# Optimization experiments

Hardware: AMD Instinct MI355X
Metric: run time of the kernel (lower is better)

Reference implementation:

```python
import jax, jax.numpy as jnp
import numpy as np
import math

SCALED = True
SUBSEQUENT_MASK = True
B, SQ, SK, D, DV = 8, 2048, 2048, 1024, 1024


def _build_mask(query_lens, key_lens, sq, sk, causal):
    # (B, Sq, Sk) boolean validity mask: rows >= q_len and cols >= k_len are masked.
    qm = jnp.arange(sq)[None, :, None] < query_lens[:, None, None]
    km = jnp.arange(sk)[None, None, :] < key_lens[:, None, None]
    mask = qm & km
    if causal:
        mask = mask & (jnp.arange(sk)[None, None, :] <= jnp.arange(sq)[None, :, None])
    return mask


def _masked_softmax(scores, mask):
    # Stable masked softmax; fully-masked rows yield exactly 0 (matches the
    # original's NaN -> 0 replacement) without producing NaNs.
    neg = jnp.finfo(scores.dtype).min
    s = jnp.where(mask, scores, neg)
    m = jnp.max(s, axis=-1, keepdims=True)
    e = jnp.where(mask, jnp.exp(s - m), jnp.zeros((), scores.dtype))
    denom = jnp.sum(e, axis=-1, keepdims=True)
    return e / jnp.where(denom == 0, jnp.ones((), scores.dtype), denom)


def setup_inputs() -> dict:
    key = jax.random.key(0)
    kq, kk, kv, kql, kkl = jax.random.split(key, 5)
    return {
        "queries": jax.random.normal(kq, (B, SQ, D), dtype=jnp.float32),
        "keys": jax.random.normal(kk, (B, SK, D), dtype=jnp.float32),
        "values": jax.random.normal(kv, (B, SK, DV), dtype=jnp.float32),
        "query_lens": jax.random.randint(kql, (B,), 1, SQ + 1),
        "key_lens": jax.random.randint(kkl, (B,), 1, SK + 1),
    }


def reference(queries, keys, values, query_lens, key_lens):
    # scores: (B, Sq, Sk)
    scores = jnp.einsum("bqd,bkd->bqk", queries, keys)
    if SCALED:
        scores = scores / math.sqrt(queries.shape[2])
    mask = _build_mask(query_lens, key_lens, queries.shape[1], keys.shape[1], SUBSEQUENT_MASK)
    weights = _masked_softmax(scores, mask)
    context = jnp.einsum("bqk,bkv->bqv", weights, values)
    return (context, weights)
```

## Files before the change

kernel.cpp:

```cpp
#include <hip/hip_runtime.h>
#include <hip/hip_bf16.h>

#define B_   8
#define SQ_  2048
#define SK_  2048
#define D_   1024
#define DV_  1024

typedef __bf16 bf16;
typedef __attribute__((ext_vector_type(4))) __bf16 bf16x4;
typedef __attribute__((ext_vector_type(8))) __bf16 bf16x8;
typedef __attribute__((ext_vector_type(4))) float  f32x4;

typedef const __attribute__((address_space(1))) void* gptr1;
typedef __attribute__((address_space(3))) void*       lptr3;

__device__ __forceinline__ void gload16(const void* g, void* l) {
    __builtin_amdgcn_global_load_lds((gptr1)g, (lptr3)l, 16, 0, 0);
}

__global__ __launch_bounds__(256)
void convert_kernel(const float* __restrict__ A, const float* __restrict__ Bm,
                    bf16* __restrict__ dA, bf16* __restrict__ dB,
                    float* __restrict__ rowsumG)
{
    if (rowsumG && blockIdx.y == 0 && blockIdx.x < 8) {
        int idx = blockIdx.x * 256 + threadIdx.x;
        float4 z = make_float4(0.f, 0.f, 0.f, 0.f);
        ((float4*)rowsumG)[idx * 2 + 0] = z;
        ((float4*)rowsumG)[idx * 2 + 1] = z;
    }
    const float* src = blockIdx.y ? Bm : A;
    bf16*        dst = blockIdx.y ? dB : dA;
    size_t i = ((size_t)blockIdx.x * 256 + threadIdx.x) * 8;
    float4 v0 = *(const float4*)(src + i);
    float4 v1 = *(const float4*)(src + i + 4);
    bf16x8 o = { (bf16)v0.x, (bf16)v0.y, (bf16)v0.z, (bf16)v0.w,
                 (bf16)v1.x, (bf16)v1.y, (bf16)v1.z, (bf16)v1.w };
    *(bf16x8*)(dst + i) = o;
}

__global__ __launch_bounds__(256)
void convVT_kernel(const float* __restrict__ V, bf16* __restrict__ VT)
{
    const int b  = blockIdx.z;
    const int k0 = blockIdx.x * 64;
    const int n0 = blockIdx.y * 64;
    __shared__ bf16 T[64][72];

    const int tid = threadIdx.x;
    #pragma unroll
    for (int i = 0; i < 4; ++i) {
        int s  = tid + i * 256;
        int r  = s >> 4;
        int c4 = (s & 15) << 2;
        float4 v = *(const float4*)(V + ((size_t)b * SK_ + (k0 + r)) * DV_ + n0 + c4);
        T[r][c4 + 0] = (bf16)v.x;
        T[r][c4 + 1] = (bf16)v.y;
        T[r][c4 + 2] = (bf16)v.z;
        T[r][c4 + 3] = (bf16)v.w;
    }
    __syncthreads();
    #pragma unroll
    for (int i = 0; i < 2; ++i) {
        int s  = tid + i * 256;
        int n  = s >> 3;
        int c8 = (s & 7) << 3;
        bf16x8 o;
        #pragma unroll
        for (int j = 0; j < 8; ++j) o[j] = T[c8 + j][n];
        *(bf16x8*)(VT + ((size_t)b * DV_ + (n0 + n)) * SK_ + k0 + c8) = o;
    }
}

__global__ __launch_bounds__(512, 4)
void scoresE_kernel(const bf16* __restrict__ Qbf, const bf16* __restrict__ Kbf,
                    const int* __restrict__ qlens, const int* __restrict__ klens,
                    bf16* __restrict__ Wbf, float* __restrict__ rowsumG)
{
    const int b  = blockIdx.z;
    const int q0 = blockIdx.y * 128;
    const int k0 = blockIdx.x * 128;
    if (k0 > q0 + 127) return;
    const int qlen = qlens[b], klen = klens[b];
    if (q0 >= qlen || k0 >= klen) return;

    __shared__ __align__(16) bf16 Qs[128][64];
    __shared__ __align__(16) bf16 Ks[128][64];
    __shared__ float rowsumL[128];

    const int tid  = threadIdx.x;
    const int lane = tid & 63;
    const int w    = tid >> 6;
    const int wq   = w >> 1, wk = w & 1;

    if (tid < 128) rowsumL[tid] = 0.f;

    const bf16* Qb = Qbf + ((size_t)b * SQ_ + q0) * D_;
    const bf16* Kb = Kbf + ((size_t)b * SK_ + k0) * D_;

    const int r0 = tid >> 3;
    const int c0 = (tid & 7) << 3;

    f32x4 acc[2][4] = {};

    for (int d0 = 0; d0 < D_; d0 += 64) {
        gload16(Qb + (size_t)r0 * D_ + d0 + c0,        &Qs[r0][c0]);
        gload16(Qb + (size_t)(r0 + 64) * D_ + d0 + c0, &Qs[r0 + 64][c0]);
        gload16(Kb + (size_t)r0 * D_ + d0 + c0,        &Ks[r0][c0]);
        gload16(Kb + (size_t)(r0 + 64) * D_ + d0 + c0, &Ks[r0 + 64][c0]);
        __syncthreads();
        #pragma unroll
        for (int kk = 0; kk < 2; ++kk) {
            const int koff = kk * 32 + ((lane >> 4) << 3);
            bf16x8 a[2], bb[4];
            #pragma unroll
            for (int m = 0; m < 2; ++m)
                a[m] = *(const bf16x8*)&Qs[32 * wq + 16 * m + (lane & 15)][koff];
            #pragma unroll
            for (int n = 0; n < 4; ++n)
                bb[n] = *(const bf16x8*)&Ks[64 * wk + 16 * n + (lane & 15)][koff];
            #pragma unroll
            for (int m = 0; m < 2; ++m)
                #pragma unroll
                for (int n = 0; n < 4; ++n)
                    acc[m][n] = __builtin_amdgcn_mfma_f32_16x16x32_bf16(a[m], bb[n], acc[m][n], 0, 0, 0);
        }
        __syncthreads();
    }

    bf16* Wrow = Wbf + ((size_t)b * SQ_ + q0) * SK_ + k0;
    const int g   = lane >> 4;
    const int cl  = lane & 15;
    const int rbl = 32 * wq + (g << 2);
    const int cbl = 64 * wk + cl;
    #pragma unroll
    for (int m = 0; m < 2; ++m) {
        #pragma unroll
        for (int r = 0; r < 4; ++r) {
            const int rl   = rbl + 16 * m + r;
            const int rowg = q0 + rl;
            float s = 0.f;
            #pragma unroll
            for (int n = 0; n < 4; ++n) {
                const int colg = k0 + cbl + 16 * n;
                float e = 0.f;
                if (rowg < qlen && colg <= rowg && colg < klen)
                    e = __expf(acc[m][n][r] * 0.03125f);
                Wrow[(size_t)rl * SK_ + cbl + 16 * n] = (bf16)e;
                s += e;
            }
            s += __shfl_xor(s, 1, 64);
            s += __shfl_xor(s, 2, 64);
            s += __shfl_xor(s, 4, 64);
            s += __shfl_xor(s, 8, 64);
            if (cl == 0) atomicAdd(&rowsumL[rl], s);
        }
    }
    __syncthreads();
    if (tid < 128) {
        float sv = rowsumL[tid];
        if (sv != 0.f) atomicAdd(&rowsumG[(size_t)b * SQ_ + q0 + tid], sv);
    }
}

__global__ __launch_bounds__(512)
void normW_kernel(const int* __restrict__ qlens, const int* __restrict__ klens,
                  const float* __restrict__ rowsumG, bf16* __restrict__ Wbf,
                  float* __restrict__ W, float* __restrict__ invG)
{
    const int b  = blockIdx.y;
    const int q0 = blockIdx.x * 64;
    const int qlen = qlens[b], klen = klens[b];
    const int tid = threadIdx.x;
    float* Wb = W + ((size_t)b * SQ_ + q0) * SK_;

    if (q0 >= qlen) {
        float4 z = make_float4(0.f, 0.f, 0.f, 0.f);
        float4* wf = (float4*)Wb;
        #pragma unroll
        for (int i = 0; i < 64; ++i) wf[tid + i * 512] = z;
        float4* bfp = (float4*)(Wbf + ((size_t)b * SQ_ + q0) * SK_);
        #pragma unroll
        for (int i = 0; i < 32; ++i) bfp[tid + i * 512] = z;
        if (tid < 64) invG[(size_t)b * SQ_ + q0 + tid] = 0.f;
        return;
    }

    const int ncols = min(klen, q0 + 64);
    const int kendB = ((ncols + 127) >> 7) << 7;

    __shared__ float invS[64];
    if (tid < 64) {
        float sv = rowsumG[(size_t)b * SQ_ + q0 + tid];
        float iv = (sv > 0.f) ? (1.f / sv) : 0.f;
        invS[tid] = iv;
        invG[(size_t)b * SQ_ + q0 + tid] = iv;
    }
    __syncthreads();

    const int r  = tid >> 3;
    const int c8 = tid & 7;
    const float iv = invS[r];
    const bf16* Erow = Wbf + ((size_t)b * SQ_ + q0 + r) * SK_;
    float* Wrow = Wb + (size_t)r * SK_;
    for (int j = 0; j < 64; ++j) {
        int col = (c8 + j * 8) << 2;
        float4 o;
        if (col < kendB) {
            bf16x4 e4 = *(const bf16x4*)&Erow[col];
            o = make_float4((float)e4[0] * iv, (float)e4[1] * iv,
                            (float)e4[2] * iv, (float)e4[3] * iv);
        } else {
            o = make_float4(0.f, 0.f, 0.f, 0.f);
        }
        *(float4*)&Wrow[col] = o;
    }
}

__global__ __launch_bounds__(512, 4)
void context_bf_kernel(const bf16* __restrict__ Wbf, const bf16* __restrict__ VT,
                       const int* __restrict__ qlens, const int* __restrict__ klens,
                       const float* __restrict__ invG, float* __restrict__ Out)
{
    const int b  = blockIdx.z;
    const int q0 = blockIdx.y * 128;
    const int n0 = blockIdx.x * 128;
    const int tid  = threadIdx.x;
    const int qlen = qlens[b];

    float* Ob = Out + (size_t)b * SQ_ * DV_;
    if (q0 >= qlen) {
        float4 z = make_float4(0.f, 0.f, 0.f, 0.f);
        #pragma unroll
        for (int i = 0; i < 8; ++i) {
            int s  = tid + i * 512;
            int r  = s >> 5;
            int c4 = (s & 31) << 2;
            *(float4*)(Ob + (size_t)(q0 + r) * DV_ + n0 + c4) = z;
        }
        return;
    }

    const int klen = klens[b];
    const int kend = min(q0 + 128, (klen + 63) & ~63);
    const int nk   = kend >> 6;

    __shared__ __align__(16) bf16 Ws[128][64];
    __shared__ __align__(16) bf16 Vs[128][64];

    const int lane = tid & 63;
    const int w    = tid >> 6;
    const int wq   = w >> 1, wn = w & 1;

    const bf16* Wb = Wbf + (size_t)b * SQ_ * SK_ + (size_t)q0 * SK_;
    const bf16* Vb = VT  + (size_t)b * DV_ * SK_ + (size_t)n0 * SK_;

    const int r0 = tid >> 3;
    const int c0 = (tid & 7) << 3;

    f32x4 acc[2][4] = {};

    for (int it = 0; it < nk; ++it) {
        const int kk0 = it * 64;
        gload16(Wb + (size_t)r0 * SK_ + kk0 + c0,        &Ws[r0][c0]);
        gload16(Wb + (size_t)(r0 + 64) * SK_ + kk0 + c0, &Ws[r0 + 64][c0]);
        gload16(Vb + (size_t)r0 * SK_ + kk0 + c0,        &Vs[r0][c0]);
        gload16(Vb + (size_t)(r0 + 64) * SK_ + kk0 + c0, &Vs[r0 + 64][c0]);
        __syncthreads();
        #pragma unroll
        for (int kk = 0; kk < 2; ++kk) {
            const int koff = kk * 32 + ((lane >> 4) << 3);
            bf16x8 a[2], bb[4];
            #pragma unroll
            for (int m = 0; m < 2; ++m)
                a[m] = *(const bf16x8*)&Ws[32 * wq + 16 * m + (lane & 15)][koff];
            #pragma unroll
            for (int n = 0; n < 4; ++n)
                bb[n] = *(const bf16x8*)&Vs[64 * wn + 16 * n + (lane & 15)][koff];
            #pragma unroll
            for (int m = 0; m < 2; ++m)
                #pragma unroll
                for (int n = 0; n < 4; ++n)
                    acc[m][n] = __builtin_amdgcn_mfma_f32_16x16x32_bf16(a[m], bb[n], acc[m][n], 0, 0, 0);
        }
        __syncthreads();
    }

    const float* invB = invG + (size_t)b * SQ_;
    const int rb = q0 + 32 * wq + ((lane >> 4) << 2);
    const int cb = n0 + 64 * wn + (lane & 15);
    #pragma unroll
    for (int m = 0; m < 2; ++m) {
        #pragma unroll
        for (int r = 0; r < 4; ++r) {
            const float iv = invB[rb + 16 * m + r];
            #pragma unroll
            for (int n = 0; n < 4; ++n)
                Ob[(size_t)(rb + 16 * m + r) * DV_ + (cb + 16 * n)] = acc[m][n][r] * iv;
        }
    }
}

__global__ __launch_bounds__(512, 4)
void scores_kernel(const float* __restrict__ Q, const float* __restrict__ K,
                   const int* __restrict__ qlens, const int* __restrict__ klens,
                   float* __restrict__ Wout)
{
    const int b  = blockIdx.z;
    const int q0 = blockIdx.y * 128;
    const int k0 = blockIdx.x * 128;
    if (k0 > q0 + 127) return;
    const int qlen = qlens[b], klen = klens[b];
    if (q0 >= qlen || k0 >= klen) return;

    __shared__ __align__(16) bf16 Qs[2][128][72];
    __shared__ __align__(16) bf16 Ks[2][128][72];

    const int tid  = threadIdx.x;
    const int lane = tid & 63;
    const int w    = tid >> 6;
    const int wq   = w >> 1, wk = w & 1;

    const float* Qb = Q + (size_t)b * SQ_ * D_;
    const float* Kb = K + (size_t)b * SK_ * D_;

    float4 qreg[4], kreg[4];
    int srow[4], sc4[4];
    #pragma unroll
    for (int i = 0; i < 4; ++i) {
        int s = tid + i * 512;
        srow[i] = s >> 4;
        sc4[i]  = (s & 15) << 2;
    }

    auto load_tile = [&](int d0) {
        #pragma unroll
        for (int i = 0; i < 4; ++i) {
            qreg[i] = *(const float4*)(Qb + (size_t)(q0 + srow[i]) * D_ + d0 + sc4[i]);
            kreg[i] = *(const float4*)(Kb + (size_t)(k0 + srow[i]) * D_ + d0 + sc4[i]);
        }
    };
    auto store_tile = [&](int buf) {
        #pragma unroll
        for (int i = 0; i < 4; ++i) {
            bf16x4 qb = { (bf16)qreg[i].x, (bf16)qreg[i].y, (bf16)qreg[i].z, (bf16)qreg[i].w };
            bf16x4 kb = { (bf16)kreg[i].x, (bf16)kreg[i].y, (bf16)kreg[i].z, (bf16)kreg[i].w };
            *(bf16x4*)&Qs[buf][srow[i]][sc4[i]] = qb;
            *(bf16x4*)&Ks[buf][srow[i]][sc4[i]] = kb;
        }
    };

    f32x4 acc[2][4] = {};
    load_tile(0);
    store_tile(0);
    __syncthreads();

    for (int it = 0; it < 16; ++it) {
        const int cur = it & 1;
        if (it < 15) load_tile((it + 1) * 64);
        #pragma unroll
        for (int kk = 0; kk < 2; ++kk) {
            const int koff = kk * 32 + ((lane >> 4) << 3);
            bf16x8 a[2], bb[4];
            #pragma unroll
            for (int m = 0; m < 2; ++m)
                a[m] = *(const bf16x8*)&Qs[cur][32 * wq + 16 * m + (lane & 15)][koff];
            #pragma unroll
            for (int n = 0; n < 4; ++n)
                bb[n] = *(const bf16x8*)&Ks[cur][64 * wk + 16 * n + (lane & 15)][koff];
            #pragma unroll
            for (int m = 0; m < 2; ++m)
                #pragma unroll
                for (int n = 0; n < 4; ++n)
                    acc[m][n] = __builtin_amdgcn_mfma_f32_16x16x32_bf16(a[m], bb[n], acc[m][n], 0, 0, 0);
        }
        if (it < 15) store_tile(1 - cur);
        __syncthreads();
    }

    float* Wb = Wout + (size_t)b * SQ_ * SK_;
    const int rb = q0 + 32 * wq + ((lane >> 4) << 2);
    const int cb = k0 + 64 * wk + (lane & 15);
    #pragma unroll
    for (int m = 0; m < 2; ++m)
        #pragma unroll
        for (int n = 0; n < 4; ++n)
            #pragma unroll
            for (int r = 0; r < 4; ++r)
                Wb[(size_t)(rb + 16 * m + r) * SK_ + (cb + 16 * n)] = acc[m][n][r] * 0.03125f;
}

__global__ __launch_bounds__(256)
void softmax_kernel(const int* __restrict__ qlens, const int* __restrict__ klens,
                    float* __restrict__ W)
{
    const int bq = blockIdx.x;
    const int b  = bq >> 11;
    const int q  = bq & 2047;
    const int qlen = qlens[b], klen = klens[b];
    int kmax = 0;
    if (q < qlen) kmax = min(klen, q + 1);

    float4* row = (float4*)(W + (size_t)bq * SK_);
    const int tid = threadIdx.x;

    float4 x[2];
    float m = -INFINITY;
    #pragma unroll
    for (int i = 0; i < 2; ++i) {
        int v4 = tid + i * 256;
        int kb = v4 << 2;
        if (kb < kmax) x[i] = row[v4];
        else           x[i] = make_float4(-INFINITY, -INFINITY, -INFINITY, -INFINITY);
        float* xe = (float*)&x[i];
        #pragma unroll
        for (int e = 0; e < 4; ++e) {
            if (kb + e >= kmax) xe[e] = -INFINITY;
            m = fmaxf(m, xe[e]);
        }
    }
    #pragma unroll
    for (int off = 32; off > 0; off >>= 1) m = fmaxf(m, __shfl_xor(m, off, 64));
    __shared__ float red[4];
    if ((tid & 63) == 0) red[tid >> 6] = m;
    __syncthreads();
    m = fmaxf(fmaxf(red[0], red[1]), fmaxf(red[2], red[3]));
    __syncthreads();

    float sum = 0.f;
    #pragma unroll
    for (int i = 0; i < 2; ++i) {
        float* xe = (float*)&x[i];
        #pragma unroll
        for (int e = 0; e < 4; ++e) {
            float ev = (xe[e] == -INFINITY) ? 0.f : __expf(xe[e] - m);
            xe[e] = ev;
            sum += ev;
        }
    }
    #pragma unroll
    for (int off = 32; off > 0; off >>= 1) sum += __shfl_xor(sum, off, 64);
    if ((tid & 63) == 0) red[tid >> 6] = sum;
    __syncthreads();
    sum = red[0] + red[1] + red[2] + red[3];

    const float inv = (sum > 0.f) ? (1.f / sum) : 0.f;
    #pragma unroll
    for (int i = 0; i < 2; ++i) {
        float* xe = (float*)&x[i];
        float4 o = { xe[0] * inv, xe[1] * inv, xe[2] * inv, xe[3] * inv };
        row[tid + i * 256] = o;
    }
}

__global__ __launch_bounds__(512, 4)
void context_kernel(const float* __restrict__ W, const float* __restrict__ V,
                    const int* __restrict__ klens, float* __restrict__ Out)
{
    const int b  = blockIdx.z;
    const int q0 = blockIdx.y * 128;
    const int n0 = blockIdx.x * 128;
    const int klen = klens[b];
    const int kend = min(q0 + 128, (klen + 63) & ~63);
    const int nk   = kend >> 6;

    __shared__ __align__(16) bf16 Ws[2][128][72];
    __shared__ __align__(16) bf16 Vs[2][128][72];

    const int tid  = threadIdx.x;
    const int lane = tid & 63;
    const int w    = tid >> 6;
    const int wq   = w >> 1, wn = w & 1;

    const float* Wb = W + (size_t)b * SQ_ * SK_;
    const float* Vb = V + (size_t)b * SK_ * DV_;

    float4 wreg[4];
    float  vreg[2][8];
    int srow[4], sc4[4], vn[2], voct[2];
    #pragma unroll
    for (int i = 0; i < 4; ++i) {
        int s = tid + i * 512;
        srow[i] = s >> 4;
        sc4[i]  = (s & 15) << 2;
    }
    #pragma unroll
    for (int i = 0; i < 2; ++i) {
        int t = tid + i * 512;
        vn[i]   = t & 127;
        voct[i] = t >> 7;
    }

    auto load_tile = [&](int kk0) {
        #pragma unroll
        for (int i = 0; i < 4; ++i)
            wreg[i] = *(const float4*)(Wb + (size_t)(q0 + srow[i]) * SK_ + kk0 + sc4[i]);
        #pragma unroll
        for (int i = 0; i < 2; ++i)
            #pragma unroll
            for (int j = 0; j < 8; ++j)
                vreg[i][j] = Vb[(size_t)(kk0 + voct[i] * 8 + j) * DV_ + n0 + vn[i]];
    };
    auto store_tile = [&](int buf) {
        #pragma unroll
        for (int i = 0; i < 4; ++i) {
            bf16x4 wb = { (bf16)wreg[i].x, (bf16)wreg[i].y, (bf16)wreg[i].z, (bf16)wreg[i].w };
            *(bf16x4*)&Ws[buf][srow[i]][sc4[i]] = wb;
        }
        #pragma unroll
        for (int i = 0; i < 2; ++i) {
            bf16x8 vb = { (bf16)vreg[i][0], (bf16)vreg[i][1], (bf16)vreg[i][2], (bf16)vreg[i][3],
                          (bf16)vreg[i][4], (bf16)vreg[i][5], (bf16)vreg[i][6], (bf16)vreg[i][7] };
            *(bf16x8*)&Vs[buf][vn[i]][voct[i] * 8] = vb;
        }
    };

    f32x4 acc[2][4] = {};
    load_tile(0);
    store_tile(0);
    __syncthreads();

    for (int it = 0; it < nk; ++it) {
        const int cur = it & 1;
        if (it + 1 < nk) load_tile((it + 1) * 64);
        #pragma unroll
        for (int kk = 0; kk < 2; ++kk) {
            const int koff = kk * 32 + ((lane >> 4) << 3);
            bf16x8 a[2], bb[4];
            #pragma unroll
            for (int m = 0; m < 2; ++m)
                a[m] = *(const bf16x8*)&Ws[cur][32 * wq + 16 * m + (lane & 15)][koff];
            #pragma unroll
            for (int n = 0; n < 4; ++n)
                bb[n] = *(const bf16x8*)&Vs[cur][64 * wn + 16 * n + (lane & 15)][koff];
            #pragma unroll
            for (int m = 0; m < 2; ++m)
                #pragma unroll
                for (int n = 0; n < 4; ++n)
                    acc[m][n] = __builtin_amdgcn_mfma_f32_16x16x32_bf16(a[m], bb[n], acc[m][n], 0, 0, 0);
        }
        if (it + 1 < nk) store_tile(1 - cur);
        __syncthreads();
    }

    float* Ob = Out + (size_t)b * SQ_ * DV_;
    const int rb = q0 + 32 * wq + ((lane >> 4) << 2);
    const int cb = n0 + 64 * wn + (lane & 15);
    #pragma unroll
    for (int m = 0; m < 2; ++m)
        #pragma unroll
        for (int n = 0; n < 4; ++n)
            #pragma unroll
            for (int r = 0; r < 4; ++r)
                Ob[(size_t)(rb + 16 * m + r) * DV_ + (cb + 16 * n)] = acc[m][n][r];
}

extern "C" void kernel_launch(void* const* d_in, const int* in_sizes, int n_in,
                              void* d_out, int out_size, void* d_ws, size_t ws_size,
                              hipStream_t stream) {
    (void)in_sizes; (void)n_in; (void)out_size;
    const float* Q     = (const float*)d_in[0];
    const float* K     = (const float*)d_in[1];
    const float* V     = (const float*)d_in[2];
    const int*   qlens = (const int*)d_in[3];
    const int*   klens = (const int*)d_in[4];

    float* ctx = (float*)d_out;
    float* wts = ctx + (size_t)B_ * SQ_ * DV_;

    const size_t nQ = (size_t)B_ * SQ_ * D_;
    const size_t nK = (size_t)B_ * SK_ * D_;
    const size_t nV = (size_t)B_ * SK_ * DV_;
    const size_t nW = (size_t)B_ * SQ_ * SK_;
    const size_t nS = (size_t)B_ * SQ_;
    const size_t ws_need = (nQ + nK + nV + nW) * sizeof(bf16) + nS * 2 * sizeof(float);

    if (d_ws && ws_size >= ws_need) {
        bf16*  qbf = (bf16*)d_ws;
        bf16*  kbf = qbf + nQ;
        bf16*  vbt = kbf + nK;
        bf16*  wbf = vbt + nV;
        float* rowsumG = (float*)(wbf + nW);
        float* invG    = rowsumG + nS;

        convert_kernel<<<dim3((unsigned)(nQ / (256 * 8)), 2), 256, 0, stream>>>(Q, K, qbf, kbf, rowsumG);
        convVT_kernel<<<dim3(SK_ / 64, DV_ / 64, B_), 256, 0, stream>>>(V, vbt);

        dim3 g1(SK_ / 128, SQ_ / 128, B_);
        scoresE_kernel<<<g1, 512, 0, stream>>>(qbf, kbf, qlens, klens, wbf, rowsumG);

        normW_kernel<<<dim3(SQ_ / 64, B_), 512, 0, stream>>>(qlens, klens, rowsumG, wbf, wts, invG);

        dim3 g3(DV_ / 128, SQ_ / 128, B_);
        context_bf_kernel<<<g3, 512, 0, stream>>>(wbf, vbt, qlens, klens, invG, ctx);
    } else {
        dim3 g1(SK_ / 128, SQ_ / 128, B_);
        scores_kernel<<<g1, 512, 0, stream>>>(Q, K, qlens, klens, wts);

        softmax_kernel<<<dim3(B_ * SQ_), 256, 0, stream>>>(qlens, klens, wts);

        dim3 g3(DV_ / 128, SQ_ / 128, B_);
        context_kernel<<<g3, 512, 0, stream>>>(wts, V, klens, ctx);
    }
}
```

Baseline: 504.8 us.

## Fuse weight normalization into context kernel and drop normW pass

Removes the separate normW kernel. The context GEMM kernel now computes inverse row sums itself into shared memory and uses them to scale its output. The blocks with n0==0 also write the normalized fp32 weights matrix, including zero-filling fully masked row tiles. This saves a kernel launch and the invG buffer, but puts the whole 1 MB weight write for each row tile on one of eight blocks, which can leave those blocks as a long tail.

```diff
diff --git a/kernel.cpp b/kernel.cpp
--- a/kernel.cpp
+++ b/kernel.cpp
@@ -164,64 +164,11 @@
     }
 }
 
-__global__ __launch_bounds__(512)
-void normW_kernel(const int* __restrict__ qlens, const int* __restrict__ klens,
-                  const float* __restrict__ rowsumG, bf16* __restrict__ Wbf,
-                  float* __restrict__ W, float* __restrict__ invG)
-{
-    const int b  = blockIdx.y;
-    const int q0 = blockIdx.x * 64;
-    const int qlen = qlens[b], klen = klens[b];
-    const int tid = threadIdx.x;
-    float* Wb = W + ((size_t)b * SQ_ + q0) * SK_;
-
-    if (q0 >= qlen) {
-        float4 z = make_float4(0.f, 0.f, 0.f, 0.f);
-        float4* wf = (float4*)Wb;
-        #pragma unroll
-        for (int i = 0; i < 64; ++i) wf[tid + i * 512] = z;
-        float4* bfp = (float4*)(Wbf + ((size_t)b * SQ_ + q0) * SK_);
-        #pragma unroll
-        for (int i = 0; i < 32; ++i) bfp[tid + i * 512] = z;
-        if (tid < 64) invG[(size_t)b * SQ_ + q0 + tid] = 0.f;
-        return;
-    }
-
-    const int ncols = min(klen, q0 + 64);
-    const int kendB = ((ncols + 127) >> 7) << 7;
-
-    __shared__ float invS[64];
-    if (tid < 64) {
-        float sv = rowsumG[(size_t)b * SQ_ + q0 + tid];
-        float iv = (sv > 0.f) ? (1.f / sv) : 0.f;
-        invS[tid] = iv;
-        invG[(size_t)b * SQ_ + q0 + tid] = iv;
-    }
-    __syncthreads();
-
-    const int r  = tid >> 3;
-    const int c8 = tid & 7;
-    const float iv = invS[r];
-    const bf16* Erow = Wbf + ((size_t)b * SQ_ + q0 + r) * SK_;
-    float* Wrow = Wb + (size_t)r * SK_;
-    for (int j = 0; j < 64; ++j) {
-        int col = (c8 + j * 8) << 2;
-        float4 o;
-        if (col < kendB) {
-            bf16x4 e4 = *(const bf16x4*)&Erow[col];
-            o = make_float4((float)e4[0] * iv, (float)e4[1] * iv,
-                            (float)e4[2] * iv, (float)e4[3] * iv);
-        } else {
-            o = make_float4(0.f, 0.f, 0.f, 0.f);
-        }
-        *(float4*)&Wrow[col] = o;
-    }
-}
-
 __global__ __launch_bounds__(512, 4)
-void context_bf_kernel(const bf16* __restrict__ Wbf, const bf16* __restrict__ VT,
-                       const int* __restrict__ qlens, const int* __restrict__ klens,
-                       const float* __restrict__ invG, float* __restrict__ Out)
+void contextW_kernel(const bf16* __restrict__ Wbf, const bf16* __restrict__ VT,
+                     const int* __restrict__ qlens, const int* __restrict__ klens,
+                     const float* __restrict__ rowsumG,
+                     float* __restrict__ Wfp, float* __restrict__ Out)
 {
     const int b  = blockIdx.z;
     const int q0 = blockIdx.y * 128;
@@ -239,6 +186,11 @@
             int c4 = (s & 31) << 2;
             *(float4*)(Ob + (size_t)(q0 + r) * DV_ + n0 + c4) = z;
         }
+        if (n0 == 0) {
+            float4* WQ = (float4*)(Wfp + ((size_t)b * SQ_ + q0) * SK_);
+            #pragma unroll 4
+            for (int i = 0; i < 128; ++i) WQ[tid + i * 512] = z;
+        }
         return;
     }
 
@@ -248,10 +200,16 @@
 
     __shared__ __align__(16) bf16 Ws[128][64];
     __shared__ __align__(16) bf16 Vs[128][64];
+    __shared__ float invS[128];
 
     const int lane = tid & 63;
     const int w    = tid >> 6;
     const int wq   = w >> 1, wn = w & 1;
+
+    if (tid < 128) {
+        float sv = rowsumG[(size_t)b * SQ_ + q0 + tid];
+        invS[tid] = (sv > 0.f) ? (1.f / sv) : 0.f;
+    }
 
     const bf16* Wb = Wbf + (size_t)b * SQ_ * SK_ + (size_t)q0 * SK_;
     const bf16* Vb = VT  + (size_t)b * DV_ * SK_ + (size_t)n0 * SK_;
@@ -287,14 +245,36 @@
         __syncthreads();
     }
 
-    const float* invB = invG + (size_t)b * SQ_;
-    const int rb = q0 + 32 * wq + ((lane >> 4) << 2);
+    if (n0 == 0) {
+        float* WQ = Wfp + ((size_t)b * SQ_ + q0) * SK_;
+        #pragma unroll 1
+        for (int j = 0; j < 64; ++j) {
+            const int gidx = j * 4096 + tid * 8;
+            const int r = gidx >> 11;
+            const int c = gidx & 2047;
+            float4 o0 = make_float4(0.f, 0.f, 0.f, 0.f);
+            float4 o1 = o0;
+            if (c < kend) {
+                const float iv = invS[r];
+                bf16x8 e = *(const bf16x8*)&Wb[(size_t)r * SK_ + c];
+                o0 = make_float4((float)e[0] * iv, (float)e[1] * iv,
+                                 (float)e[2] * iv, (float)e[3] * iv);
+                o1 = make_float4((float)e[4] * iv, (float)e[5] * iv,
+                                 (float)e[6] * iv, (float)e[7] * iv);
+            }
+            *(float4*)&WQ[(size_t)r * SK_ + c]     = o0;
+            *(float4*)&WQ[(size_t)r * SK_ + c + 4] = o1;
+        }
+    }
+
+    const int rbl = 32 * wq + ((lane >> 4) << 2);
+    const int rb = q0 + rbl;
     const int cb = n0 + 64 * wn + (lane & 15);
     #pragma unroll
     for (int m = 0; m < 2; ++m) {
         #pragma unroll
         for (int r = 0; r < 4; ++r) {
-            const float iv = invB[rb + 16 * m + r];
+            const float iv = invS[rbl + 16 * m + r];
             #pragma unroll
             for (int n = 0; n < 4; ++n)
                 Ob[(size_t)(rb + 16 * m + r) * DV_ + (cb + 16 * n)] = acc[m][n][r] * iv;
@@ -574,7 +554,7 @@
     const size_t nV = (size_t)B_ * SK_ * DV_;
     const size_t nW = (size_t)B_ * SQ_ * SK_;
     const size_t nS = (size_t)B_ * SQ_;
-    const size_t ws_need = (nQ + nK + nV + nW) * sizeof(bf16) + nS * 2 * sizeof(float);
+    const size_t ws_need = (nQ + nK + nV + nW) * sizeof(bf16) + nS * sizeof(float);
 
     if (d_ws && ws_size >= ws_need) {
         bf16*  qbf = (bf16*)d_ws;
@@ -582,7 +562,6 @@
         bf16*  vbt = kbf + nK;
         bf16*  wbf = vbt + nV;
         float* rowsumG = (float*)(wbf + nW);
-        float* invG    = rowsumG + nS;
 
         convert_kernel<<<dim3((unsigned)(nQ / (256 * 8)), 2), 256, 0, stream>>>(Q, K, qbf, kbf, rowsumG);
         convVT_kernel<<<dim3(SK_ / 64, DV_ / 64, B_), 256, 0, stream>>>(V, vbt);
@@ -590,10 +569,8 @@
         dim3 g1(SK_ / 128, SQ_ / 128, B_);
         scoresE_kernel<<<g1, 512, 0, stream>>>(qbf, kbf, qlens, klens, wbf, rowsumG);
 
-        normW_kernel<<<dim3(SQ_ / 64, B_), 512, 0, stream>>>(qlens, klens, rowsumG, wbf, wts, invG);
-
         dim3 g3(DV_ / 128, SQ_ / 128, B_);
-        context_bf_kernel<<<g3, 512, 0, stream>>>(wbf, vbt, qlens, klens, invG, ctx);
+        contextW_kernel<<<g3, 512, 0, stream>>>(wbf, vbt, qlens, klens, rowsumG, wts, ctx);
     } else {
         dim3 g1(SK_ / 128, SQ_ / 128, B_);
         scores_kernel<<<g1, 512, 0, stream>>>(Q, K, qlens, klens, wts);
```

After: 572.2 us. 1.13x slower.
